# Optimization experiments

Hardware: AMD Instinct MI355X
Metric: run time of the kernel (lower is better)

Reference implementation:

```python
import jax, jax.numpy as jnp
import numpy as np

EPS_MSG = 1e-7   # GENConv eps added after ReLU on messages
LN_EPS = 1e-5    # torch LayerNorm default eps
N_NODES = 100000
N_EDGES = 1200000
NODE_DIM = 128
EDGE_DIM = 8
HID = 64
OUT_DIM = 112
L = 7            # num_layers


def layer_norm(x, g, b):
    mu = jnp.mean(x, axis=-1, keepdims=True)
    var = jnp.mean((x - mu) ** 2, axis=-1, keepdims=True)
    return (x - mu) * jax.lax.rsqrt(var + LN_EPS) * g + b


def setup_inputs() -> dict:
    key = jax.random.key(0)
    ks = jax.random.split(key, 10)
    return {
        "node_feats": jax.random.normal(ks[0], (N_NODES, NODE_DIM), jnp.float32),
        "edge_feats": jax.random.normal(ks[1], (N_EDGES, EDGE_DIM), jnp.float32),
        "src": jax.random.randint(ks[2], (N_EDGES,), 0, N_NODES, dtype=jnp.int32),
        "dst": jax.random.randint(ks[3], (N_EDGES,), 0, N_NODES, dtype=jnp.int32),
        "W_node": (jax.random.normal(ks[4], (NODE_DIM, HID), jnp.float32) * 0.05),
        "b_node": jnp.zeros((HID,), jnp.float32),
        "W_edge": (jax.random.normal(ks[5], (EDGE_DIM, HID), jnp.float32) * 0.05),
        "b_edge": jnp.zeros((HID,), jnp.float32),
        "betas": jnp.ones((L,), jnp.float32),  # learnable beta per GENConv, init 1.0
        "W1": (jax.random.normal(ks[6], (L, HID, 2 * HID), jnp.float32) * 0.05),
        "b1": jnp.zeros((L, 2 * HID), jnp.float32),
        "ln1_g": jnp.ones((L, 2 * HID), jnp.float32),
        "ln1_b": jnp.zeros((L, 2 * HID), jnp.float32),
        "W2": (jax.random.normal(ks[7], (L, 2 * HID, HID), jnp.float32) * 0.05),
        "b2": jnp.zeros((L, HID), jnp.float32),
        "norm_g": jnp.ones((L, HID), jnp.float32),   # DeepGCNLayer LayerNorm affine
        "norm_b": jnp.zeros((L, HID), jnp.float32),
        "W_out": (jax.random.normal(ks[8], (HID, OUT_DIM), jnp.float32) * 0.05),
        "b_out": jnp.zeros((OUT_DIM,), jnp.float32),
    }


def reference(node_feats, edge_feats, src, dst, W_node, b_node, W_edge, b_edge,
              betas, W1, b1, ln1_g, ln1_b, W2, b2, norm_g, norm_b, W_out, b_out):
    h = node_feats @ W_node + b_node        # [N, HID] node encoder
    eh = edge_feats @ W_edge + b_edge       # [E, HID] edge encoder
    for i in range(L):
        # DeepGCNLayer 'res+': x = dropout(relu(norm(h))); h = h + conv(x)
        # (dropout is identity in eval mode)
        x = jax.nn.relu(layer_norm(h, norm_g[i], norm_b[i]))
        # GENConv softmax aggregation with learnable beta
        m = jax.nn.relu(x[src] + eh) + EPS_MSG          # [E, HID] messages
        logits = m * betas[i]
        mx = jax.ops.segment_max(logits, dst, num_segments=N_NODES)
        e = jnp.exp(logits - mx[dst])
        s = jax.ops.segment_sum(e, dst, num_segments=N_NODES)
        a = e / s[dst]                                   # per-dst per-feature softmax
        agg = jax.ops.segment_sum(m * a, dst, num_segments=N_NODES)  # [N, HID]
        # GENConv MLP (2 layers, HID -> 2*HID -> HID, LayerNorm+ReLU in between)
        y = x + agg
        y = jax.nn.relu(layer_norm(y @ W1[i] + b1[i], ln1_g[i], ln1_b[i]))
        y = y @ W2[i] + b2[i]
        h = h + y
    # final: activation(norm_of_layer0(h)) -> dropout(identity) -> output linear
    h = jax.nn.relu(layer_norm(h, norm_g[0], norm_b[0]))
    return h @ W_out + b_out
```

## Files before the change

### kernel.cpp

```cpp
#include <hip/hip_runtime.h>
#include <hip/hip_bf16.h>

#define N_NODES 100000
#define N_PAD   100032
#define N_EDGES 1200000
#define HID 64
#define OUT_DIM 112
#define NLAYERS 7

static constexpr int SCAN_BLOCKS = (N_NODES + 255) / 256;

typedef __attribute__((ext_vector_type(8))) short short8v;
typedef __attribute__((ext_vector_type(4))) float f32x4;
typedef unsigned int uint;
typedef unsigned short ushort;

__device__ __forceinline__ unsigned f2b(float f) {
    unsigned u = __builtin_bit_cast(unsigned, f);
    return (u + 0x7FFFu + ((u >> 16) & 1u)) >> 16;
}
__device__ __forceinline__ float blo(uint v) {
    return __builtin_bit_cast(float, (v & 0xFFFFu) << 16);
}
__device__ __forceinline__ float bhi(uint v) {
    return __builtin_bit_cast(float, v & 0xFFFF0000u);
}


__global__ __launch_bounds__(256) void k_hist(const int* __restrict__ dst, int* __restrict__ cnt) {
    int e0 = (blockIdx.x * 256 + threadIdx.x) * 4;
    if (e0 + 3 < N_EDGES) {
        int4 d4 = *(const int4*)&dst[e0];
        atomicAdd(&cnt[d4.x], 1);
        atomicAdd(&cnt[d4.y], 1);
        atomicAdd(&cnt[d4.z], 1);
        atomicAdd(&cnt[d4.w], 1);
    } else {
        for (int e = e0; e < N_EDGES; ++e) atomicAdd(&cnt[dst[e]], 1);
    }
}

__global__ __launch_bounds__(256) void k_scan_a(const int* __restrict__ cnt, int* __restrict__ inc,
                                                int* __restrict__ bsum) {
    __shared__ int lds[4];
    int i = blockIdx.x * 256 + threadIdx.x;
    int v = (i < N_NODES) ? cnt[i] : 0;
    int lane = threadIdx.x & 63, w = threadIdx.x >> 6;
    #pragma unroll
    for (int d = 1; d < 64; d <<= 1) {
        int u = __shfl_up(v, d, 64);
        if (lane >= d) v += u;
    }
    if (lane == 63) lds[w] = v;
    __syncthreads();
    int add = 0;
    for (int j = 0; j < w; ++j) add += lds[j];
    v += add;
    if (i < N_NODES) inc[i] = v;
    if (threadIdx.x == 255) bsum[blockIdx.x] = v;
}

__global__ __launch_bounds__(512) void k_scan_b(const int* __restrict__ bsum, int* __restrict__ boff, int nb) {
    __shared__ int lds[8];
    int t = threadIdx.x;
    int v0 = (t < nb) ? bsum[t] : 0;
    int v = v0;
    int lane = t & 63, w = t >> 6;
    #pragma unroll
    for (int d = 1; d < 64; d <<= 1) {
        int u = __shfl_up(v, d, 64);
        if (lane >= d) v += u;
    }
    if (lane == 63) lds[w] = v;
    __syncthreads();
    int add = 0;
    for (int j = 0; j < w; ++j) add += lds[j];
    boff[t] = v + add - v0;
}

__global__ __launch_bounds__(256) void k_scan_c(const int* __restrict__ inc, const int* __restrict__ boff,
                                                int* __restrict__ rp) {
    int i = blockIdx.x * 256 + threadIdx.x;
    if (i < N_NODES) {
        rp[i + 1] = inc[i] + boff[blockIdx.x];
        if (i == 0) rp[0] = 0;
    }
}

__global__ __launch_bounds__(256) void k_scatter(const int* __restrict__ src, const int* __restrict__ dst,
                                                 int* __restrict__ nxt, int* __restrict__ ssrc,
                                                 int* __restrict__ pos) {
    int e0 = (blockIdx.x * 256 + threadIdx.x) * 4;
    if (e0 + 3 < N_EDGES) {
        int4 d4 = *(const int4*)&dst[e0];
        int4 s4 = *(const int4*)&src[e0];
        int p0 = atomicAdd(&nxt[d4.x], 1);
        int p1 = atomicAdd(&nxt[d4.y], 1);
        int p2 = atomicAdd(&nxt[d4.z], 1);
        int p3 = atomicAdd(&nxt[d4.w], 1);
        ssrc[p0] = s4.x;
        ssrc[p1] = s4.y;
        ssrc[p2] = s4.z;
        ssrc[p3] = s4.w;
        *(int4*)&pos[e0] = make_int4(p0, p1, p2, p3);
    } else {
        for (int e = e0; e < N_EDGES; ++e) {
            int p = atomicAdd(&nxt[dst[e]], 1);
            ssrc[p] = src[e];
            pos[e] = p;
        }
    }
}

__global__ __launch_bounds__(256) void k_prep_w(const float* __restrict__ W1, const float* __restrict__ W2,
                                                const float* __restrict__ Wn, const float* __restrict__ Wo,
                                                short* __restrict__ W1T, short* __restrict__ W2T,
                                                short* __restrict__ WnT, short* __restrict__ WoT) {
    int t = blockIdx.x * 256 + threadIdx.x;
    if (t < NLAYERS * 8192) {
        int l = t >> 13, r = t & 8191;
        int o1 = r >> 6, k1 = r & 63;
        W1T[t] = (short)f2b(W1[l * 8192 + k1 * 128 + o1]);
        int o2 = r >> 7, k2 = r & 127;
        W2T[t] = (short)f2b(W2[l * 8192 + k2 * 64 + o2]);
        if (t < 8192) {
            int o = t >> 7, k = t & 127;
            WnT[t] = (short)f2b(Wn[k * 64 + o]);
        }
        if (t < OUT_DIM * 64) {
            int o = t >> 6, k = t & 63;
            WoT[t] = (short)f2b(Wo[k * OUT_DIM + o]);
        }
    }
}


__global__ __launch_bounds__(256) void k_node_enc_mfma(
    const float* __restrict__ nf, const short* __restrict__ WnT, const float* __restrict__ bn,
    const float* __restrict__ g, const float* __restrict__ b,
    float* __restrict__ h, float* __restrict__ x, ushort* __restrict__ xb) {
    __shared__ __align__(16) short Wns[8192];
    __shared__ __align__(16) short nfs[4][2048];
    int tid = threadIdx.x, lane = tid & 63, w = tid >> 6;

    {
        const int4* gp = (const int4*)WnT;
        for (int u = tid; u < 1024; u += 256) {
            int byte = u * 16;
            int off = byte ^ (((byte >> 8) & 7) << 4);
            *(int4*)((char*)Wns + off) = gp[u];
        }
    }
    int nbase = blockIdx.x * 64 + w * 16;
    #pragma unroll
    for (int it = 0; it < 8; ++it) {
        int idx = it * 256 + lane * 4;
        int node = idx >> 7, k0 = idx & 127;
        int gn = nbase + node;
        float4 v = (gn < N_NODES) ? *(const float4*)&nf[(size_t)gn * 128 + k0]
                                  : make_float4(0.f, 0.f, 0.f, 0.f);
        uint2 pk;
        pk.x = f2b(v.x) | (f2b(v.y) << 16);
        pk.y = f2b(v.z) | (f2b(v.w) << 16);
        int boff = (node * 256 + k0 * 2) ^ ((node & 7) << 4);
        *(uint2*)((char*)nfs[w] + boff) = pk;
    }
    __syncthreads();

    int cg = lane >> 4, cl = lane & 15;
    float bv[4], gv[4], bbv[4];
    #pragma unroll
    for (int t = 0; t < 4; ++t) {
        bv[t] = bn[t * 16 + cl]; gv[t] = g[t * 16 + cl]; bbv[t] = b[t * 16 + cl];
    }
    f32x4 c[4];
    #pragma unroll
    for (int t = 0; t < 4; ++t) c[t] = (f32x4){bv[t], bv[t], bv[t], bv[t]};
    #pragma unroll
    for (int s = 0; s < 4; ++s) {
        int aoff = (cl * 256 + s * 64 + cg * 16) ^ ((cl & 7) << 4);
        short8v af = *(const short8v*)((char*)nfs[w] + aoff);
        #pragma unroll
        for (int t = 0; t < 4; ++t) {
            int o = t * 16 + cl;
            int boff = (o * 256 + s * 64 + cg * 16) ^ ((o & 7) << 4);
            short8v bfv = *(const short8v*)((char*)Wns + boff);
            c[t] = __builtin_amdgcn_mfma_f32_16x16x32_bf16(af, bfv, c[t], 0, 0, 0);
        }
    }
    float s2[4] = {0, 0, 0, 0}, q2[4] = {0, 0, 0, 0};
    #pragma unroll
    for (int t = 0; t < 4; ++t)
        #pragma unroll
        for (int r = 0; r < 4; ++r) {
            int node = nbase + cg * 4 + r, o = t * 16 + cl;
            h[(size_t)node * 64 + o] = c[t][r];
            s2[r] += c[t][r]; q2[r] += c[t][r] * c[t][r];
        }
    #pragma unroll
    for (int r = 0; r < 4; ++r)
        #pragma unroll
        for (int d = 1; d < 16; d <<= 1) {
            s2[r] += __shfl_xor(s2[r], d, 16);
            q2[r] += __shfl_xor(q2[r], d, 16);
        }
    #pragma unroll
    for (int r = 0; r < 4; ++r) {
        float mu = s2[r] * (1.f / 64.f);
        float var = q2[r] * (1.f / 64.f) - mu * mu;
        float rv = rsqrtf(var + 1e-5f);
        #pragma unroll
        for (int t = 0; t < 4; ++t) {
            int node = nbase + cg * 4 + r, o = t * 16 + cl;
            float xv = fmaxf((c[t][r] - mu) * rv * gv[t] + bbv[t], 0.f);
            x[(size_t)node * 64 + o] = xv;
            xb[(size_t)node * 64 + o] = (ushort)f2b(xv);
        }
    }
}

__global__ __launch_bounds__(256) void k_edge_enc(const float* __restrict__ ef, const float* __restrict__ We,
                                                  const float* __restrict__ be, const int* __restrict__ pos,
                                                  ushort* __restrict__ eh) {
    __shared__ float efs[2048];
    int tid = threadIdx.x, lane = tid & 63, w = tid >> 6;
    float wreg[8];
    #pragma unroll
    for (int k = 0; k < 8; ++k) wreg[k] = We[k * 64 + lane];
    float bv = be[lane];
    int base = blockIdx.x * 256;
    if (base >= N_EDGES) return;
    #pragma unroll
    for (int u = 0; u < 2; ++u) {
        int idx = u * 1024 + tid * 4;
        size_t gidx = (size_t)base * 8 + idx;
        float4 v = (gidx < (size_t)N_EDGES * 8) ? *(const float4*)&ef[gidx]
                                                : make_float4(0.f, 0.f, 0.f, 0.f);
        *(float4*)&efs[idx] = v;
    }
    int ge0 = base + w * 64 + lane;
    int myp = (ge0 < N_EDGES) ? pos[ge0] : -1;
    __syncthreads();
    #pragma unroll 4
    for (int j = 0; j < 64; ++j) {
        int p = __shfl(myp, j, 64);
        if (p >= 0) {
            float4 a = *(const float4*)&efs[(w * 64 + j) * 8];
            float4 b = *(const float4*)&efs[(w * 64 + j) * 8 + 4];
            float acc = bv;
            acc = fmaf(a.x, wreg[0], acc); acc = fmaf(a.y, wreg[1], acc);
            acc = fmaf(a.z, wreg[2], acc); acc = fmaf(a.w, wreg[3], acc);
            acc = fmaf(b.x, wreg[4], acc); acc = fmaf(b.y, wreg[5], acc);
            acc = fmaf(b.z, wreg[6], acc); acc = fmaf(b.w, wreg[7], acc);
            eh[(size_t)p * 64 + lane] = (ushort)f2b(acc);
        }
    }
}


__global__ __launch_bounds__(256) void k_agg(
    const float* __restrict__ x, const ushort* __restrict__ xb,
    const ushort* __restrict__ eh, const int* __restrict__ ssrc,
    const int* __restrict__ rp, const float* __restrict__ betas, int layer,
    ushort* __restrict__ xab) {
    int lane = threadIdx.x & 63;
    int n = blockIdx.x * 8 + (threadIdx.x >> 6) * 2 + (lane >> 5);
    int slot = (lane >> 3) & 3;
    int f8 = lane & 7;
    float beta = betas[layer];
    int r0 = rp[n], r1 = rp[n + 1];
    float S[8], T[8];
    #pragma unroll
    for (int c = 0; c < 8; ++c) { S[c] = 0.f; T[c] = 0.f; }
    int i = r0 + slot;
    for (; i + 4 < r1; i += 8) {
        int sA = ssrc[i], sB = ssrc[i + 4];
        uint4 xvA = *(const uint4*)&xb[(size_t)sA * 64 + 8 * f8];
        uint4 evA = *(const uint4*)&eh[(size_t)i * 64 + 8 * f8];
        uint4 xvB = *(const uint4*)&xb[(size_t)sB * 64 + 8 * f8];
        uint4 evB = *(const uint4*)&eh[(size_t)(i + 4) * 64 + 8 * f8];
        float mA[8], mB[8];
        mA[0] = fmaxf(blo(xvA.x) + blo(evA.x), 0.f) + 1e-7f;
        mA[1] = fmaxf(bhi(xvA.x) + bhi(evA.x), 0.f) + 1e-7f;
        mA[2] = fmaxf(blo(xvA.y) + blo(evA.y), 0.f) + 1e-7f;
        mA[3] = fmaxf(bhi(xvA.y) + bhi(evA.y), 0.f) + 1e-7f;
        mA[4] = fmaxf(blo(xvA.z) + blo(evA.z), 0.f) + 1e-7f;
        mA[5] = fmaxf(bhi(xvA.z) + bhi(evA.z), 0.f) + 1e-7f;
        mA[6] = fmaxf(blo(xvA.w) + blo(evA.w), 0.f) + 1e-7f;
        mA[7] = fmaxf(bhi(xvA.w) + bhi(evA.w), 0.f) + 1e-7f;
        mB[0] = fmaxf(blo(xvB.x) + blo(evB.x), 0.f) + 1e-7f;
        mB[1] = fmaxf(bhi(xvB.x) + bhi(evB.x), 0.f) + 1e-7f;
        mB[2] = fmaxf(blo(xvB.y) + blo(evB.y), 0.f) + 1e-7f;
        mB[3] = fmaxf(bhi(xvB.y) + bhi(evB.y), 0.f) + 1e-7f;
        mB[4] = fmaxf(blo(xvB.z) + blo(evB.z), 0.f) + 1e-7f;
        mB[5] = fmaxf(bhi(xvB.z) + bhi(evB.z), 0.f) + 1e-7f;
        mB[6] = fmaxf(blo(xvB.w) + blo(evB.w), 0.f) + 1e-7f;
        mB[7] = fmaxf(bhi(xvB.w) + bhi(evB.w), 0.f) + 1e-7f;
        #pragma unroll
        for (int c = 0; c < 8; ++c) {
            float pA = __expf(mA[c] * beta);
            float pB = __expf(mB[c] * beta);
            S[c] += pA + pB;
            T[c] += mA[c] * pA + mB[c] * pB;
        }
    }
    for (; i < r1; i += 4) {
        int s0 = ssrc[i];
        uint4 xv = *(const uint4*)&xb[(size_t)s0 * 64 + 8 * f8];
        uint4 ev = *(const uint4*)&eh[(size_t)i * 64 + 8 * f8];
        float m[8];
        m[0] = fmaxf(blo(xv.x) + blo(ev.x), 0.f) + 1e-7f;
        m[1] = fmaxf(bhi(xv.x) + bhi(ev.x), 0.f) + 1e-7f;
        m[2] = fmaxf(blo(xv.y) + blo(ev.y), 0.f) + 1e-7f;
        m[3] = fmaxf(bhi(xv.y) + bhi(ev.y), 0.f) + 1e-7f;
        m[4] = fmaxf(blo(xv.z) + blo(ev.z), 0.f) + 1e-7f;
        m[5] = fmaxf(bhi(xv.z) + bhi(ev.z), 0.f) + 1e-7f;
        m[6] = fmaxf(blo(xv.w) + blo(ev.w), 0.f) + 1e-7f;
        m[7] = fmaxf(bhi(xv.w) + bhi(ev.w), 0.f) + 1e-7f;
        #pragma unroll
        for (int c = 0; c < 8; ++c) {
            float p = __expf(m[c] * beta);
            S[c] += p;
            T[c] += m[c] * p;
        }
    }
    #pragma unroll
    for (int c = 0; c < 8; ++c) {
        #pragma unroll
        for (int d = 8; d <= 16; d <<= 1) {
            S[c] += __shfl_xor(S[c], d, 64);
            T[c] += __shfl_xor(T[c], d, 64);
        }
    }
    if (slot == 0) {
        bool has = r1 > r0;
        float a[8];
        #pragma unroll
        for (int c = 0; c < 8; ++c) a[c] = has ? (T[c] / S[c]) : 0.f;
        float4 xv0 = *(const float4*)&x[(size_t)n * 64 + 8 * f8];
        float4 xv1 = *(const float4*)&x[(size_t)n * 64 + 8 * f8 + 4];
        uint4 pk;
        pk.x = f2b(xv0.x + a[0]) | (f2b(xv0.y + a[1]) << 16);
        pk.y = f2b(xv0.z + a[2]) | (f2b(xv0.w + a[3]) << 16);
        pk.z = f2b(xv1.x + a[4]) | (f2b(xv1.y + a[5]) << 16);
        pk.w = f2b(xv1.z + a[6]) | (f2b(xv1.w + a[7]) << 16);
        *(uint4*)&xab[(size_t)n * 64 + 8 * f8] = pk;
    }
}

__global__ __launch_bounds__(256) void k_mlp_mfma(
    const ushort* __restrict__ xab, const short* __restrict__ W1T, const float* __restrict__ b1,
    const float* __restrict__ g1, const float* __restrict__ bt1,
    const short* __restrict__ W2T, const float* __restrict__ b2,
    const float* __restrict__ ng, const float* __restrict__ nb,
    float* __restrict__ h, float* __restrict__ xout, ushort* __restrict__ xbout) {
    __shared__ __align__(16) short W1s[8192];
    __shared__ __align__(16) short W2s[8192];
    __shared__ __align__(16) short xas[4][1024];
    __shared__ __align__(16) short t1s[4][2048];
    int tid = threadIdx.x;
    int lane = tid & 63, w = tid >> 6;

    {
        const int4* g1p = (const int4*)W1T;
        const int4* g2p = (const int4*)W2T;
        for (int u = tid; u < 1024; u += 256) {
            int byte = u * 16;
            int off1 = byte ^ ((((byte >> 7) & 7)) << 4);
            *(int4*)((char*)W1s + off1) = g1p[u];
            int off2 = byte ^ ((((byte >> 8) & 7)) << 4);
            *(int4*)((char*)W2s + off2) = g2p[u];
        }
    }
    int nbase = blockIdx.x * 64 + w * 16;
    #pragma unroll
    for (int it = 0; it < 2; ++it) {
        int idx = it * 512 + lane * 8;
        int node = idx >> 6, k0 = idx & 63;
        int4 v = *(const int4*)&xab[(size_t)(nbase + node) * 64 + k0];
        int boff = (node * 128 + k0 * 2) ^ ((node & 7) << 4);
        *(int4*)((char*)xas[w] + boff) = v;
    }
    __syncthreads();

    int cg = lane >> 4;
    int cl = lane & 15;
    float b1v[8], g1v[8], t1bv[8];
    #pragma unroll
    for (int t = 0; t < 8; ++t) {
        b1v[t] = b1[t * 16 + cl]; g1v[t] = g1[t * 16 + cl]; t1bv[t] = bt1[t * 16 + cl];
    }
    f32x4 c1[8];
    #pragma unroll
    for (int t = 0; t < 8; ++t) c1[t] = (f32x4){b1v[t], b1v[t], b1v[t], b1v[t]};
    #pragma unroll
    for (int s = 0; s < 2; ++s) {
        int aoff = (cl * 128 + s * 64 + cg * 16) ^ ((cl & 7) << 4);
        short8v af = *(const short8v*)((char*)xas[w] + aoff);
        #pragma unroll
        for (int t = 0; t < 8; ++t) {
            int o = t * 16 + cl;
            int boff = (o * 128 + s * 64 + cg * 16) ^ ((o & 7) << 4);
            short8v bfv = *(const short8v*)((char*)W1s + boff);
            c1[t] = __builtin_amdgcn_mfma_f32_16x16x32_bf16(af, bfv, c1[t], 0, 0, 0);
        }
    }
    float sum[4] = {0, 0, 0, 0}, sq[4] = {0, 0, 0, 0};
    #pragma unroll
    for (int t = 0; t < 8; ++t)
        #pragma unroll
        for (int r = 0; r < 4; ++r) { sum[r] += c1[t][r]; sq[r] += c1[t][r] * c1[t][r]; }
    #pragma unroll
    for (int r = 0; r < 4; ++r)
        #pragma unroll
        for (int d = 1; d < 16; d <<= 1) {
            sum[r] += __shfl_xor(sum[r], d, 16);
            sq[r] += __shfl_xor(sq[r], d, 16);
        }
    float mu[4], rs[4];
    #pragma unroll
    for (int r = 0; r < 4; ++r) {
        mu[r] = sum[r] * (1.f / 128.f);
        float var = sq[r] * (1.f / 128.f) - mu[r] * mu[r];
        rs[r] = rsqrtf(var + 1e-5f);
    }
    #pragma unroll
    for (int t = 0; t < 8; ++t)
        #pragma unroll
        for (int r = 0; r < 4; ++r) {
            float v = fmaxf((c1[t][r] - mu[r]) * rs[r] * g1v[t] + t1bv[t], 0.f);
            int node = cg * 4 + r, o = t * 16 + cl;
            int boff = (node * 256 + o * 2) ^ ((node & 7) << 4);
            *(short*)((char*)t1s[w] + boff) = (short)f2b(v);
        }
    __syncthreads();
    float b2v[4], ngv[4], nbv[4];
    #pragma unroll
    for (int t = 0; t < 4; ++t) {
        b2v[t] = b2[t * 16 + cl]; ngv[t] = ng[t * 16 + cl]; nbv[t] = nb[t * 16 + cl];
    }
    f32x4 c2[4];
    #pragma unroll
    for (int t = 0; t < 4; ++t) c2[t] = (f32x4){b2v[t], b2v[t], b2v[t], b2v[t]};
    #pragma unroll
    for (int s = 0; s < 4; ++s) {
        int aoff = (cl * 256 + s * 64 + cg * 16) ^ ((cl & 7) << 4);
        short8v af = *(const short8v*)((char*)t1s[w] + aoff);
        #pragma unroll
        for (int t = 0; t < 4; ++t) {
            int o = t * 16 + cl;
            int boff = (o * 256 + s * 64 + cg * 16) ^ ((o & 7) << 4);
            short8v bfv = *(const short8v*)((char*)W2s + boff);
            c2[t] = __builtin_amdgcn_mfma_f32_16x16x32_bf16(af, bfv, c2[t], 0, 0, 0);
        }
    }
    float hv[4][4];
    #pragma unroll
    for (int t = 0; t < 4; ++t)
        #pragma unroll
        for (int r = 0; r < 4; ++r) {
            int node = nbase + cg * 4 + r, o = t * 16 + cl;
            float v = h[(size_t)node * 64 + o] + c2[t][r];
            h[(size_t)node * 64 + o] = v;
            hv[t][r] = v;
        }
    float s2[4] = {0, 0, 0, 0}, q2[4] = {0, 0, 0, 0};
    #pragma unroll
    for (int t = 0; t < 4; ++t)
        #pragma unroll
        for (int r = 0; r < 4; ++r) { s2[r] += hv[t][r]; q2[r] += hv[t][r] * hv[t][r]; }
    #pragma unroll
    for (int r = 0; r < 4; ++r)
        #pragma unroll
        for (int d = 1; d < 16; d <<= 1) {
            s2[r] += __shfl_xor(s2[r], d, 16);
            q2[r] += __shfl_xor(q2[r], d, 16);
        }
    #pragma unroll
    for (int r = 0; r < 4; ++r) {
        float m2 = s2[r] * (1.f / 64.f);
        float var = q2[r] * (1.f / 64.f) - m2 * m2;
        float rv = rsqrtf(var + 1e-5f);
        #pragma unroll
        for (int t = 0; t < 4; ++t) {
            int node = nbase + cg * 4 + r, o = t * 16 + cl;
            float xv = fmaxf((hv[t][r] - m2) * rv * ngv[t] + nbv[t], 0.f);
            xout[(size_t)node * 64 + o] = xv;
            xbout[(size_t)node * 64 + o] = (ushort)f2b(xv);
        }
    }
}

__global__ __launch_bounds__(256) void k_out_mfma(
    const ushort* __restrict__ xb, const short* __restrict__ WoT, const float* __restrict__ bo,
    float* __restrict__ out) {
    __shared__ __align__(16) short Wos[OUT_DIM * 64];
    __shared__ __align__(16) short xs[4][1024];
    int tid = threadIdx.x, lane = tid & 63, w = tid >> 6;

    {
        const int4* gp = (const int4*)WoT;
        for (int u = tid; u < OUT_DIM * 8; u += 256) {
            int byte = u * 16;
            int off = byte ^ (((byte >> 7) & 7) << 4);
            *(int4*)((char*)Wos + off) = gp[u];
        }
    }
    int nbase = blockIdx.x * 64 + w * 16;
    #pragma unroll
    for (int it = 0; it < 2; ++it) {
        int idx = it * 512 + lane * 8;
        int node = idx >> 6, k0 = idx & 63;
        int4 v = *(const int4*)&xb[(size_t)(nbase + node) * 64 + k0];
        int boff = (node * 128 + k0 * 2) ^ ((node & 7) << 4);
        *(int4*)((char*)xs[w] + boff) = v;
    }
    __syncthreads();

    int cg = lane >> 4, cl = lane & 15;
    f32x4 c[7];
    #pragma unroll
    for (int t = 0; t < 7; ++t) {
        float bv = bo[t * 16 + cl];
        c[t] = (f32x4){bv, bv, bv, bv};
    }
    #pragma unroll
    for (int s = 0; s < 2; ++s) {
        int aoff = (cl * 128 + s * 64 + cg * 16) ^ ((cl & 7) << 4);
        short8v af = *(const short8v*)((char*)xs[w] + aoff);
        #pragma unroll
        for (int t = 0; t < 7; ++t) {
            int o = t * 16 + cl;
            int boff = (o * 128 + s * 64 + cg * 16) ^ ((o & 7) << 4);
            short8v bfv = *(const short8v*)((char*)Wos + boff);
            c[t] = __builtin_amdgcn_mfma_f32_16x16x32_bf16(af, bfv, c[t], 0, 0, 0);
        }
    }
    #pragma unroll
    for (int t = 0; t < 7; ++t)
        #pragma unroll
        for (int r = 0; r < 4; ++r) {
            int node = nbase + cg * 4 + r;
            if (node < N_NODES) out[(size_t)node * OUT_DIM + t * 16 + cl] = c[t][r];
        }
}


extern "C" void kernel_launch(void* const* d_in, const int* in_sizes, int n_in,
                              void* d_out, int out_size, void* d_ws, size_t ws_size,
                              hipStream_t stream) {
    (void)in_sizes; (void)n_in; (void)out_size; (void)ws_size;
    const float* node_feats = (const float*)d_in[0];
    const float* edge_feats = (const float*)d_in[1];
    const int*   src        = (const int*)d_in[2];
    const int*   dst        = (const int*)d_in[3];
    const float* W_node     = (const float*)d_in[4];
    const float* b_node     = (const float*)d_in[5];
    const float* W_edge     = (const float*)d_in[6];
    const float* b_edge     = (const float*)d_in[7];
    const float* betas      = (const float*)d_in[8];
    const float* W1         = (const float*)d_in[9];
    const float* b1         = (const float*)d_in[10];
    const float* ln1_g      = (const float*)d_in[11];
    const float* ln1_b      = (const float*)d_in[12];
    const float* W2         = (const float*)d_in[13];
    const float* b2         = (const float*)d_in[14];
    const float* norm_g     = (const float*)d_in[15];
    const float* norm_b     = (const float*)d_in[16];
    const float* W_out      = (const float*)d_in[17];
    const float* b_out      = (const float*)d_in[18];
    float* out = (float*)d_out;

    char* p = (char*)d_ws;
    auto carve = [&](size_t bytes) {
        char* r = p;
        p += (bytes + 255) & ~(size_t)255;
        return r;
    };
    float*  h   = (float*)carve((size_t)N_PAD * 64 * sizeof(float));
    float*  x   = (float*)carve((size_t)N_PAD * 64 * sizeof(float));
    ushort* xb  = (ushort*)carve((size_t)N_PAD * 64 * sizeof(short));
    ushort* xab = (ushort*)carve((size_t)N_PAD * 64 * sizeof(short));
    ushort* eh  = (ushort*)carve((size_t)N_EDGES * 64 * sizeof(short));
    int* rp   = (int*)carve((size_t)(N_NODES + 1) * sizeof(int));
    int* nxt  = (int*)carve((size_t)N_NODES * sizeof(int));
    int* inc  = (int*)carve((size_t)N_NODES * sizeof(int));
    int* ssrc = (int*)carve((size_t)N_EDGES * sizeof(int));
    int* pos  = (int*)carve((size_t)N_EDGES * sizeof(int));
    int* bsum = (int*)carve(512 * sizeof(int));
    int* boff = (int*)carve(512 * sizeof(int));
    short* W1T = (short*)carve((size_t)NLAYERS * 8192 * sizeof(short));
    short* W2T = (short*)carve((size_t)NLAYERS * 8192 * sizeof(short));
    short* WnT = (short*)carve((size_t)8192 * sizeof(short));
    short* WoT = (short*)carve((size_t)OUT_DIM * 64 * sizeof(short));

    hipMemsetAsync(nxt, 0, (size_t)N_NODES * sizeof(int), stream);
    k_hist<<<(N_EDGES / 4 + 255) / 256, 256, 0, stream>>>(dst, nxt);
    k_scan_a<<<SCAN_BLOCKS, 256, 0, stream>>>(nxt, inc, bsum);
    k_scan_b<<<1, 512, 0, stream>>>(bsum, boff, SCAN_BLOCKS);
    k_scan_c<<<SCAN_BLOCKS, 256, 0, stream>>>(inc, boff, rp);
    hipMemcpyAsync(nxt, rp, (size_t)N_NODES * sizeof(int), hipMemcpyDeviceToDevice, stream);
    k_scatter<<<(N_EDGES / 4 + 255) / 256, 256, 0, stream>>>(src, dst, nxt, ssrc, pos);

    k_prep_w<<<(NLAYERS * 8192 + 255) / 256, 256, 0, stream>>>(W1, W2, W_node, W_out,
                                                               W1T, W2T, WnT, WoT);
    k_node_enc_mfma<<<N_PAD / 64, 256, 0, stream>>>(node_feats, WnT, b_node, norm_g, norm_b, h, x, xb);
    k_edge_enc<<<(N_EDGES + 255) / 256, 256, 0, stream>>>(edge_feats, W_edge, b_edge, pos, eh);

    for (int i = 0; i < NLAYERS; ++i) {
        int ni = (i + 1 < NLAYERS) ? (i + 1) : 0;
        k_agg<<<N_NODES / 8, 256, 0, stream>>>(x, xb, eh, ssrc, rp, betas, i, xab);
        k_mlp_mfma<<<N_PAD / 64, 256, 0, stream>>>(xab, W1T + i * 8192, b1 + i * 128,
                                                   ln1_g + i * 128, ln1_b + i * 128,
                                                   W2T + i * 8192, b2 + i * 64,
                                                   norm_g + ni * 64, norm_b + ni * 64,
                                                   h, x, xb);
    }

    k_out_mfma<<<N_PAD / 64, 256, 0, stream>>>(xb, WoT, b_out, out);
}
```

Baseline: 791.7 us.

## Derive CSR slots from histogram ranks and drop fp32 activation copy

The histogram kernel now records each edge's atomic rank within its destination. The edge encoder computes the CSR position as rp[dst]+rank and scatters src itself, which removes the separate scatter kernel, its second pass of atomics and the device copy. The fp32 copy of x is also dropped: the aggregation reads the bf16 xb for the residual x term, so each layer no longer writes and reads 64 floats per node. In exchange the residual x is now added at bf16 precision rather than fp32, which slightly changes numerics.

```diff
diff --git a/kernel.cpp b/kernel.cpp
--- a/kernel.cpp
+++ b/kernel.cpp
@@ -27,16 +27,18 @@
 }
 
 
-__global__ __launch_bounds__(256) void k_hist(const int* __restrict__ dst, int* __restrict__ cnt) {
+__global__ __launch_bounds__(256) void k_rank(const int* __restrict__ dst, int* __restrict__ cnt,
+                                              int* __restrict__ rank) {
     int e0 = (blockIdx.x * 256 + threadIdx.x) * 4;
     if (e0 + 3 < N_EDGES) {
         int4 d4 = *(const int4*)&dst[e0];
-        atomicAdd(&cnt[d4.x], 1);
-        atomicAdd(&cnt[d4.y], 1);
-        atomicAdd(&cnt[d4.z], 1);
-        atomicAdd(&cnt[d4.w], 1);
+        int r0 = atomicAdd(&cnt[d4.x], 1);
+        int r1 = atomicAdd(&cnt[d4.y], 1);
+        int r2 = atomicAdd(&cnt[d4.z], 1);
+        int r3 = atomicAdd(&cnt[d4.w], 1);
+        *(int4*)&rank[e0] = make_int4(r0, r1, r2, r3);
     } else {
-        for (int e = e0; e < N_EDGES; ++e) atomicAdd(&cnt[dst[e]], 1);
+        for (int e = e0; e < N_EDGES; ++e) rank[e] = atomicAdd(&cnt[dst[e]], 1);
     }
 }
 
@@ -84,31 +86,6 @@
     if (i < N_NODES) {
         rp[i + 1] = inc[i] + boff[blockIdx.x];
         if (i == 0) rp[0] = 0;
-    }
-}
-
-__global__ __launch_bounds__(256) void k_scatter(const int* __restrict__ src, const int* __restrict__ dst,
-                                                 int* __restrict__ nxt, int* __restrict__ ssrc,
-                                                 int* __restrict__ pos) {
-    int e0 = (blockIdx.x * 256 + threadIdx.x) * 4;
-    if (e0 + 3 < N_EDGES) {
-        int4 d4 = *(const int4*)&dst[e0];
-        int4 s4 = *(const int4*)&src[e0];
-        int p0 = atomicAdd(&nxt[d4.x], 1);
-        int p1 = atomicAdd(&nxt[d4.y], 1);
-        int p2 = atomicAdd(&nxt[d4.z], 1);
-        int p3 = atomicAdd(&nxt[d4.w], 1);
-        ssrc[p0] = s4.x;
-        ssrc[p1] = s4.y;
-        ssrc[p2] = s4.z;
-        ssrc[p3] = s4.w;
-        *(int4*)&pos[e0] = make_int4(p0, p1, p2, p3);
-    } else {
-        for (int e = e0; e < N_EDGES; ++e) {
-            int p = atomicAdd(&nxt[dst[e]], 1);
-            ssrc[p] = src[e];
-            pos[e] = p;
-        }
     }
 }
 
@@ -138,7 +115,7 @@
 __global__ __launch_bounds__(256) void k_node_enc_mfma(
     const float* __restrict__ nf, const short* __restrict__ WnT, const float* __restrict__ bn,
     const float* __restrict__ g, const float* __restrict__ b,
-    float* __restrict__ h, float* __restrict__ x, ushort* __restrict__ xb) {
+    float* __restrict__ h, ushort* __restrict__ xb) {
     __shared__ __align__(16) short Wns[8192];
     __shared__ __align__(16) short nfs[4][2048];
     int tid = threadIdx.x, lane = tid & 63, w = tid >> 6;
@@ -213,15 +190,15 @@
         for (int t = 0; t < 4; ++t) {
             int node = nbase + cg * 4 + r, o = t * 16 + cl;
             float xv = fmaxf((c[t][r] - mu) * rv * gv[t] + bbv[t], 0.f);
-            x[(size_t)node * 64 + o] = xv;
             xb[(size_t)node * 64 + o] = (ushort)f2b(xv);
         }
     }
 }
 
-__global__ __launch_bounds__(256) void k_edge_enc(const float* __restrict__ ef, const float* __restrict__ We,
-                                                  const float* __restrict__ be, const int* __restrict__ pos,
-                                                  ushort* __restrict__ eh) {
+__global__ __launch_bounds__(256) void k_edge_enc(
+    const float* __restrict__ ef, const float* __restrict__ We, const float* __restrict__ be,
+    const int* __restrict__ dst, const int* __restrict__ rank, const int* __restrict__ rp,
+    const int* __restrict__ src, int* __restrict__ ssrc, ushort* __restrict__ eh) {
     __shared__ float efs[2048];
     int tid = threadIdx.x, lane = tid & 63, w = tid >> 6;
     float wreg[8];
@@ -239,7 +216,11 @@
         *(float4*)&efs[idx] = v;
     }
     int ge0 = base + w * 64 + lane;
-    int myp = (ge0 < N_EDGES) ? pos[ge0] : -1;
+    int myp = -1;
+    if (ge0 < N_EDGES) {
+        myp = rp[dst[ge0]] + rank[ge0];
+        ssrc[myp] = src[ge0];
+    }
     __syncthreads();
     #pragma unroll 4
     for (int j = 0; j < 64; ++j) {
@@ -259,10 +240,9 @@
 
 
 __global__ __launch_bounds__(256) void k_agg(
-    const float* __restrict__ x, const ushort* __restrict__ xb,
-    const ushort* __restrict__ eh, const int* __restrict__ ssrc,
-    const int* __restrict__ rp, const float* __restrict__ betas, int layer,
-    ushort* __restrict__ xab) {
+    const ushort* __restrict__ xb, const ushort* __restrict__ eh,
+    const int* __restrict__ ssrc, const int* __restrict__ rp,
+    const float* __restrict__ betas, int layer, ushort* __restrict__ xab) {
     int lane = threadIdx.x & 63;
     int n = blockIdx.x * 8 + (threadIdx.x >> 6) * 2 + (lane >> 5);
     int slot = (lane >> 3) & 3;
@@ -337,13 +317,12 @@
         float a[8];
         #pragma unroll
         for (int c = 0; c < 8; ++c) a[c] = has ? (T[c] / S[c]) : 0.f;
-        float4 xv0 = *(const float4*)&x[(size_t)n * 64 + 8 * f8];
-        float4 xv1 = *(const float4*)&x[(size_t)n * 64 + 8 * f8 + 4];
+        uint4 xv = *(const uint4*)&xb[(size_t)n * 64 + 8 * f8];
         uint4 pk;
-        pk.x = f2b(xv0.x + a[0]) | (f2b(xv0.y + a[1]) << 16);
-        pk.y = f2b(xv0.z + a[2]) | (f2b(xv0.w + a[3]) << 16);
-        pk.z = f2b(xv1.x + a[4]) | (f2b(xv1.y + a[5]) << 16);
-        pk.w = f2b(xv1.z + a[6]) | (f2b(xv1.w + a[7]) << 16);
+        pk.x = f2b(blo(xv.x) + a[0]) | (f2b(bhi(xv.x) + a[1]) << 16);
+        pk.y = f2b(blo(xv.y) + a[2]) | (f2b(bhi(xv.y) + a[3]) << 16);
+        pk.z = f2b(blo(xv.z) + a[4]) | (f2b(bhi(xv.z) + a[5]) << 16);
+        pk.w = f2b(blo(xv.w) + a[6]) | (f2b(bhi(xv.w) + a[7]) << 16);
         *(uint4*)&xab[(size_t)n * 64 + 8 * f8] = pk;
     }
 }
@@ -353,7 +332,7 @@
     const float* __restrict__ g1, const float* __restrict__ bt1,
     const short* __restrict__ W2T, const float* __restrict__ b2,
     const float* __restrict__ ng, const float* __restrict__ nb,
-    float* __restrict__ h, float* __restrict__ xout, ushort* __restrict__ xbout) {
+    float* __restrict__ h, ushort* __restrict__ xbout) {
     __shared__ __align__(16) short W1s[8192];
     __shared__ __align__(16) short W2s[8192];
     __shared__ __align__(16) short xas[4][1024];
@@ -485,7 +464,6 @@
         for (int t = 0; t < 4; ++t) {
             int node = nbase + cg * 4 + r, o = t * 16 + cl;
             float xv = fmaxf((hv[t][r] - m2) * rv * ngv[t] + nbv[t], 0.f);
-            xout[(size_t)node * 64 + o] = xv;
             xbout[(size_t)node * 64 + o] = (ushort)f2b(xv);
         }
     }
@@ -577,16 +555,15 @@
         p += (bytes + 255) & ~(size_t)255;
         return r;
     };
-    float*  h   = (float*)carve((size_t)N_PAD * 64 * sizeof(float));
-    float*  x   = (float*)carve((size_t)N_PAD * 64 * sizeof(float));
-    ushort* xb  = (ushort*)carve((size_t)N_PAD * 64 * sizeof(short));
-    ushort* xab = (ushort*)carve((size_t)N_PAD * 64 * sizeof(short));
-    ushort* eh  = (ushort*)carve((size_t)N_EDGES * 64 * sizeof(short));
+    float*  h    = (float*)carve((size_t)N_PAD * 64 * sizeof(float));
+    ushort* xb   = (ushort*)carve((size_t)N_PAD * 64 * sizeof(short));
+    ushort* xab  = (ushort*)carve((size_t)N_PAD * 64 * sizeof(short));
+    ushort* eh   = (ushort*)carve((size_t)N_EDGES * 64 * sizeof(short));
     int* rp   = (int*)carve((size_t)(N_NODES + 1) * sizeof(int));
     int* nxt  = (int*)carve((size_t)N_NODES * sizeof(int));
     int* inc  = (int*)carve((size_t)N_NODES * sizeof(int));
     int* ssrc = (int*)carve((size_t)N_EDGES * sizeof(int));
-    int* pos  = (int*)carve((size_t)N_EDGES * sizeof(int));
+    int* rank = (int*)carve((size_t)N_EDGES * sizeof(int));
     int* bsum = (int*)carve(512 * sizeof(int));
     int* boff = (int*)carve(512 * sizeof(int));
     short* W1T = (short*)carve((size_t)NLAYERS * 8192 * sizeof(short));
@@ -595,26 +572,25 @@
     short* WoT = (short*)carve((size_t)OUT_DIM * 64 * sizeof(short));
 
     hipMemsetAsync(nxt, 0, (size_t)N_NODES * sizeof(int), stream);
-    k_hist<<<(N_EDGES / 4 + 255) / 256, 256, 0, stream>>>(dst, nxt);
+    k_rank<<<(N_EDGES / 4 + 255) / 256, 256, 0, stream>>>(dst, nxt, rank);
     k_scan_a<<<SCAN_BLOCKS, 256, 0, stream>>>(nxt, inc, bsum);
     k_scan_b<<<1, 512, 0, stream>>>(bsum, boff, SCAN_BLOCKS);
     k_scan_c<<<SCAN_BLOCKS, 256, 0, stream>>>(inc, boff, rp);
-    hipMemcpyAsync(nxt, rp, (size_t)N_NODES * sizeof(int), hipMemcpyDeviceToDevice, stream);
-    k_scatter<<<(N_EDGES / 4 + 255) / 256, 256, 0, stream>>>(src, dst, nxt, ssrc, pos);
 
     k_prep_w<<<(NLAYERS * 8192 + 255) / 256, 256, 0, stream>>>(W1, W2, W_node, W_out,
                                                                W1T, W2T, WnT, WoT);
-    k_node_enc_mfma<<<N_PAD / 64, 256, 0, stream>>>(node_feats, WnT, b_node, norm_g, norm_b, h, x, xb);
-    k_edge_enc<<<(N_EDGES + 255) / 256, 256, 0, stream>>>(edge_feats, W_edge, b_edge, pos, eh);
+    k_node_enc_mfma<<<N_PAD / 64, 256, 0, stream>>>(node_feats, WnT, b_node, norm_g, norm_b, h, xb);
+    k_edge_enc<<<(N_EDGES + 255) / 256, 256, 0, stream>>>(edge_feats, W_edge, b_edge,
+                                                          dst, rank, rp, src, ssrc, eh);
 
     for (int i = 0; i < NLAYERS; ++i) {
         int ni = (i + 1 < NLAYERS) ? (i + 1) : 0;
-        k_agg<<<N_NODES / 8, 256, 0, stream>>>(x, xb, eh, ssrc, rp, betas, i, xab);
+        k_agg<<<N_NODES / 8, 256, 0, stream>>>(xb, eh, ssrc, rp, betas, i, xab);
         k_mlp_mfma<<<N_PAD / 64, 256, 0, stream>>>(xab, W1T + i * 8192, b1 + i * 128,
                                                    ln1_g + i * 128, ln1_b + i * 128,
                                                    W2T + i * 8192, b2 + i * 64,
                                                    norm_g + ni * 64, norm_b + ni * 64,
-                                                   h, x, xb);
+                                                   h, xb);
     }
 
     k_out_mfma<<<N_PAD / 64, 256, 0, stream>>>(xb, WoT, b_out, out);
```

Measured after the change: 717.3 us. 9.4% less time.
